# Kernel optimization log

Measured on AMD Instinct MI355X. Metric: run time of the kernel, lower is better.

Reference implementation:

```python
import jax, jax.numpy as jnp
import numpy as np

B, D, R, E, L = 8192, 2048, 64, 4, 3


def setup_inputs() -> dict:
    key = jax.random.key(0)
    ks = jax.random.split(key, 6)
    inputs = jax.random.normal(ks[0], (B, D), dtype=jnp.float32)
    # xavier-normal-ish init for low-rank factors
    U = jax.random.normal(ks[1], (L, E, D, R), dtype=jnp.float32) * (2.0 / (D + R)) ** 0.5
    V = jax.random.normal(ks[2], (L, E, D, R), dtype=jnp.float32) * (2.0 / (D + R)) ** 0.5
    C = jax.random.normal(ks[3], (L, E, R, R), dtype=jnp.float32) * (1.0 / R) ** 0.5
    gate_w = jax.random.normal(ks[4], (E, D), dtype=jnp.float32) * (1.0 / D) ** 0.5
    bias = jnp.zeros((L, D), dtype=jnp.float32)
    return {"inputs": inputs, "U": U, "V": V, "C": C, "gate_w": gate_w, "bias": bias}


def reference(inputs, U, V, C, gate_w, bias):
    x0 = inputs                      # (B, D)
    x_l = inputs
    for i in range(L):
        # gating scores per expert, softmax over experts
        gs = jax.nn.softmax(x_l @ gate_w.T, axis=-1)            # (B, E)
        # low-rank cross: tanh(V^T x) -> tanh(C .) -> U .
        vx = jnp.tanh(jnp.einsum('edr,bd->ber', V[i], x_l))     # (B, E, R)
        cx = jnp.tanh(jnp.einsum('esr,ber->bes', C[i], vx))     # (B, E, R)
        uv = jnp.einsum('eds,bes->bed', U[i], cx)               # (B, E, D)
        dot = (uv + bias[i][None, None, :]) * x0[:, None, :]    # (B, E, D)
        x_l = jnp.einsum('bed,be->bd', dot, gs) + x_l           # MoE combine + residual
    return x_l
```

## Files before the change

### kernel.cpp

```cpp
#include <hip/hip_runtime.h>
#include <cmath>

#define Bb 8192
#define Dd 2048
#define Rr 64
#define Ee 4
#define Ll 3

typedef __bf16 bf16x8 __attribute__((ext_vector_type(8)));
typedef float f32x4 __attribute__((ext_vector_type(4)));
typedef unsigned short u16x8 __attribute__((ext_vector_type(8)));
typedef unsigned short u16x4 __attribute__((ext_vector_type(4)));

__device__ __forceinline__ unsigned short f2bf(float f){
  unsigned u = __builtin_bit_cast(unsigned, f);
  u += 0x7fffu + ((u >> 16) & 1u);
  return (unsigned short)(u >> 16);
}
__device__ __forceinline__ float bf2f(unsigned short h){
  return __builtin_bit_cast(float, ((unsigned)h) << 16);
}

__global__ __launch_bounds__(256) void prep_w_k(const float* __restrict__ U,
                                                const float* __restrict__ V,
                                                const float* __restrict__ C,
                                                const float* __restrict__ gw,
                                                unsigned short* __restrict__ VfT,
                                                unsigned short* __restrict__ UfT,
                                                unsigned short* __restrict__ cb16,
                                                unsigned short* __restrict__ gw16){
  const int NV = Ll * 256 * Dd;
  const int NU = Ll * Dd * 256;
  const int NC = Ll * Ee * Rr * Rr;
  const int NG = Ee * Dd;
  const int total = NV + NU + NC + NG;
  for (int idx = blockIdx.x * blockDim.x + threadIdx.x; idx < total; idx += gridDim.x * blockDim.x){
    if (idx < NV){
      int l = idx / (256 * Dd); int rem = idx - l * 256 * Dd;
      int n = rem / Dd, d = rem - n * Dd;
      int e = n >> 6, r = n & 63;
      VfT[idx] = f2bf(V[(((size_t)l * Ee + e) * Dd + d) * Rr + r]);
    } else if (idx < NV + NU){
      int j = idx - NV;
      int l = j / (Dd * 256); int rem = j - l * Dd * 256;
      int d = rem / 256, k = rem - d * 256;
      int e = k >> 6, s = k & 63;
      UfT[j] = f2bf(U[(((size_t)l * Ee + e) * Dd + d) * Rr + s]);
    } else if (idx < NV + NU + NC){
      int j = idx - NV - NU;
      cb16[j] = f2bf(C[j]);
    } else {
      int j = idx - NV - NU - NC;
      gw16[j] = f2bf(gw[j]);
    }
  }
}

__global__ __launch_bounds__(256) void cast_gate_k(const float* __restrict__ x,
                                                   unsigned short* __restrict__ xb0,
                                                   const unsigned short* __restrict__ gw16,
                                                   float* __restrict__ gs){
  const int lane = threadIdx.x & 63;
  const int w = threadIdx.x >> 6;
  const int row = blockIdx.x * 4 + w;
  float s0 = 0.f, s1 = 0.f, s2 = 0.f, s3 = 0.f;
  #pragma unroll
  for (int c = 0; c < 4; c++){
    const int k = c * 512 + lane * 8;
    const float* xr = x + (size_t)row * Dd + k;
    f32x4 v0 = *(const f32x4*)xr;
    f32x4 v1 = *(const f32x4*)(xr + 4);
    float xf[8];
    u16x8 ob;
    #pragma unroll
    for (int u = 0; u < 4; u++){
      xf[u] = v0[u]; xf[4 + u] = v1[u];
      ob[u] = f2bf(v0[u]); ob[4 + u] = f2bf(v1[u]);
    }
    *(u16x8*)(xb0 + (size_t)row * Dd + k) = ob;
    u16x8 g0v = *(const u16x8*)(gw16 + 0 * Dd + k);
    u16x8 g1v = *(const u16x8*)(gw16 + 1 * Dd + k);
    u16x8 g2v = *(const u16x8*)(gw16 + 2 * Dd + k);
    u16x8 g3v = *(const u16x8*)(gw16 + 3 * Dd + k);
    #pragma unroll
    for (int u = 0; u < 8; u++){
      s0 += xf[u] * bf2f(g0v[u]);
      s1 += xf[u] * bf2f(g1v[u]);
      s2 += xf[u] * bf2f(g2v[u]);
      s3 += xf[u] * bf2f(g3v[u]);
    }
  }
  #pragma unroll
  for (int m = 1; m < 64; m <<= 1){
    s0 += __shfl_xor(s0, m, 64);
    s1 += __shfl_xor(s1, m, 64);
    s2 += __shfl_xor(s2, m, 64);
    s3 += __shfl_xor(s3, m, 64);
  }
  if (lane == 0){
    float mx = fmaxf(fmaxf(s0, s1), fmaxf(s2, s3));
    float e0 = __expf(s0 - mx), e1 = __expf(s1 - mx), e2 = __expf(s2 - mx), e3 = __expf(s3 - mx);
    float inv = 1.f / (e0 + e1 + e2 + e3);
    f32x4 g; g[0] = e0 * inv; g[1] = e1 * inv; g[2] = e2 * inv; g[3] = e3 * inv;
    *(f32x4*)(gs + (size_t)row * 4) = g;
  }
}

__global__ __launch_bounds__(256) void gate_k(const float* __restrict__ xv,
                                              const unsigned short* __restrict__ gw16,
                                              float* __restrict__ gs){
  const int lane = threadIdx.x & 63;
  const int w = threadIdx.x >> 6;
  const int row = blockIdx.x * 4 + w;
  float s0 = 0.f, s1 = 0.f, s2 = 0.f, s3 = 0.f;
  #pragma unroll
  for (int c = 0; c < 4; c++){
    const int k = c * 512 + lane * 8;
    const float* xr = xv + (size_t)row * Dd + k;
    f32x4 v0 = *(const f32x4*)xr;
    f32x4 v1 = *(const f32x4*)(xr + 4);
    float xf[8];
    #pragma unroll
    for (int u = 0; u < 4; u++){ xf[u] = v0[u]; xf[4 + u] = v1[u]; }
    u16x8 g0v = *(const u16x8*)(gw16 + 0 * Dd + k);
    u16x8 g1v = *(const u16x8*)(gw16 + 1 * Dd + k);
    u16x8 g2v = *(const u16x8*)(gw16 + 2 * Dd + k);
    u16x8 g3v = *(const u16x8*)(gw16 + 3 * Dd + k);
    #pragma unroll
    for (int u = 0; u < 8; u++){
      s0 += xf[u] * bf2f(g0v[u]);
      s1 += xf[u] * bf2f(g1v[u]);
      s2 += xf[u] * bf2f(g2v[u]);
      s3 += xf[u] * bf2f(g3v[u]);
    }
  }
  #pragma unroll
  for (int m = 1; m < 64; m <<= 1){
    s0 += __shfl_xor(s0, m, 64);
    s1 += __shfl_xor(s1, m, 64);
    s2 += __shfl_xor(s2, m, 64);
    s3 += __shfl_xor(s3, m, 64);
  }
  if (lane == 0){
    float mx = fmaxf(fmaxf(s0, s1), fmaxf(s2, s3));
    float e0 = __expf(s0 - mx), e1 = __expf(s1 - mx), e2 = __expf(s2 - mx), e3 = __expf(s3 - mx);
    float inv = 1.f / (e0 + e1 + e2 + e3);
    f32x4 g; g[0] = e0 * inv; g[1] = e1 * inv; g[2] = e2 * inv; g[3] = e3 * inv;
    *(f32x4*)(gs + (size_t)row * 4) = g;
  }
}

template<bool AF32>
__global__ __launch_bounds__(256) void gemm1_k(const void* __restrict__ Av,
                                               const unsigned short* __restrict__ BT,
                                               unsigned short* __restrict__ vxp){
  const int bm0 = blockIdx.x * 128;
  const int bn0 = blockIdx.y * 128;
  const int z   = blockIdx.z;
  const int kc0 = z * 512;
  const int tid = threadIdx.x;
  const int lane = tid & 63;
  const int wv = tid >> 6;
  const int wm = wv >> 1, wn = wv & 1;

  __shared__ __align__(16) char smraw[20480];
  unsigned short (*As)[40] = (unsigned short (*)[40])smraw;
  unsigned short (*Bs)[40] = (unsigned short (*)[40])(smraw + 10240);
  float (*epi)[132] = (float (*)[132])smraw;

  f32x4 acc[4][4] = {};
  const int arow = tid >> 2;
  const int aseg = tid & 3;

  const float* Af = (const float*)Av;
  const unsigned short* Ab = (const unsigned short*)Av;

  f32x4 a4[4]; u16x8 ar0, ar1;
  u16x8 br0, br1;
  if constexpr (AF32){
    a4[0] = *(const f32x4*)(Af + (size_t)(bm0 + arow) * Dd + kc0 + aseg * 8);
    a4[1] = *(const f32x4*)(Af + (size_t)(bm0 + arow) * Dd + kc0 + aseg * 8 + 4);
    a4[2] = *(const f32x4*)(Af + (size_t)(bm0 + arow + 64) * Dd + kc0 + aseg * 8);
    a4[3] = *(const f32x4*)(Af + (size_t)(bm0 + arow + 64) * Dd + kc0 + aseg * 8 + 4);
  } else {
    ar0 = *(const u16x8*)(Ab + (size_t)(bm0 + arow) * Dd + kc0 + aseg * 8);
    ar1 = *(const u16x8*)(Ab + (size_t)(bm0 + arow + 64) * Dd + kc0 + aseg * 8);
  }
  br0 = *(const u16x8*)(BT + (size_t)(bn0 + arow) * Dd + kc0 + aseg * 8);
  br1 = *(const u16x8*)(BT + (size_t)(bn0 + arow + 64) * Dd + kc0 + aseg * 8);

  for (int k0 = kc0; k0 < kc0 + 512; k0 += 32){
    __syncthreads();
    if constexpr (AF32){
      u16x8 av0, av1;
      #pragma unroll
      for (int j = 0; j < 4; j++){
        av0[j] = f2bf(a4[0][j]); av0[4 + j] = f2bf(a4[1][j]);
        av1[j] = f2bf(a4[2][j]); av1[4 + j] = f2bf(a4[3][j]);
      }
      *(u16x8*)(&As[arow][aseg * 8])      = av0;
      *(u16x8*)(&As[arow + 64][aseg * 8]) = av1;
    } else {
      *(u16x8*)(&As[arow][aseg * 8])      = ar0;
      *(u16x8*)(&As[arow + 64][aseg * 8]) = ar1;
    }
    *(u16x8*)(&Bs[arow][aseg * 8])      = br0;
    *(u16x8*)(&Bs[arow + 64][aseg * 8]) = br1;
    __syncthreads();

    int kn = k0 + 32;
    if (kn < kc0 + 512){
      if constexpr (AF32){
        a4[0] = *(const f32x4*)(Af + (size_t)(bm0 + arow) * Dd + kn + aseg * 8);
        a4[1] = *(const f32x4*)(Af + (size_t)(bm0 + arow) * Dd + kn + aseg * 8 + 4);
        a4[2] = *(const f32x4*)(Af + (size_t)(bm0 + arow + 64) * Dd + kn + aseg * 8);
        a4[3] = *(const f32x4*)(Af + (size_t)(bm0 + arow + 64) * Dd + kn + aseg * 8 + 4);
      } else {
        ar0 = *(const u16x8*)(Ab + (size_t)(bm0 + arow) * Dd + kn + aseg * 8);
        ar1 = *(const u16x8*)(Ab + (size_t)(bm0 + arow + 64) * Dd + kn + aseg * 8);
      }
      br0 = *(const u16x8*)(BT + (size_t)(bn0 + arow) * Dd + kn + aseg * 8);
      br1 = *(const u16x8*)(BT + (size_t)(bn0 + arow + 64) * Dd + kn + aseg * 8);
    }

    bf16x8 af[4];
    #pragma unroll
    for (int mi = 0; mi < 4; mi++)
      af[mi] = *reinterpret_cast<const bf16x8*>(&As[wm * 64 + mi * 16 + (lane & 15)][(lane >> 4) * 8]);
    #pragma unroll
    for (int nj = 0; nj < 4; nj++){
      bf16x8 bfr = *reinterpret_cast<const bf16x8*>(&Bs[wn * 64 + nj * 16 + (lane & 15)][(lane >> 4) * 8]);
      #pragma unroll
      for (int mi = 0; mi < 4; mi++)
        acc[mi][nj] = __builtin_amdgcn_mfma_f32_16x16x32_bf16(af[mi], bfr, acc[mi][nj], 0, 0, 0);
    }
  }

  unsigned short* outz = vxp + (size_t)z * Bb * 256;
  #pragma unroll
  for (int h = 0; h < 4; h++){
    __syncthreads();
    if (wm == (h >> 1)){
      const int mib = (h & 1) * 2;
      #pragma unroll
      for (int m2 = 0; m2 < 2; m2++)
        #pragma unroll
        for (int nj = 0; nj < 4; nj++)
          #pragma unroll
          for (int q = 0; q < 4; q++)
            epi[m2 * 16 + (lane >> 4) * 4 + q][wn * 64 + nj * 16 + (lane & 15)] = acc[mib + m2][nj][q];
    }
    __syncthreads();
    #pragma unroll
    for (int c = 0; c < 2; c++){
      int idx = c * 256 + tid;
      int r = idx >> 4;
      int col = (idx & 15) * 8;
      f32x4 v0 = *(const f32x4*)&epi[r][col];
      f32x4 v1 = *(const f32x4*)&epi[r][col + 4];
      u16x8 ov;
      #pragma unroll
      for (int j = 0; j < 4; j++){ ov[j] = f2bf(v0[j]); ov[4 + j] = f2bf(v1[j]); }
      *(u16x8*)(outz + (size_t)(bm0 + h * 32 + r) * 256 + bn0 + col) = ov;
    }
  }
}

template<bool FROMPLOG>
__global__ __launch_bounds__(256) void gemm2_k(const unsigned short* __restrict__ vxp,
                                               const unsigned short* __restrict__ cb,
                                               const float* __restrict__ gsb,
                                               const float* __restrict__ plog,
                                               unsigned short* __restrict__ wb){
  const int bm0 = blockIdx.x * 64;
  const int e   = blockIdx.y;
  const int tid = threadIdx.x;
  const int lane = tid & 63;
  const int wv = tid >> 6;
  const int wm = wv >> 1, wn = wv & 1;

  __shared__ __align__(16) char smraw[19456];
  unsigned short (*As)[72] = (unsigned short (*)[72])smraw;
  unsigned short (*Bs)[72] = (unsigned short (*)[72])(smraw + 9216);
  float (*gs_l)[4] = (float (*)[4])(smraw + 18432);
  unsigned short (*epi)[72] = (unsigned short (*)[72])smraw;

  if constexpr (FROMPLOG){
    int r = tid >> 2, q = tid & 3;
    f32x4 s = {0.f, 0.f, 0.f, 0.f};
    #pragma unroll
    for (int ci = 0; ci < 4; ci++)
      s += *(const f32x4*)(plog + ((size_t)(q * 4 + ci) * Bb + bm0 + r) * 4);
    #pragma unroll
    for (int j = 0; j < 4; j++){
      s[j] += __shfl_xor(s[j], 1, 64);
      s[j] += __shfl_xor(s[j], 2, 64);
    }
    if (q == 0){
      float mx = fmaxf(fmaxf(s[0], s[1]), fmaxf(s[2], s[3]));
      float e0 = __expf(s[0] - mx), e1 = __expf(s[1] - mx), e2 = __expf(s[2] - mx), e3 = __expf(s[3] - mx);
      float inv = 1.f / (e0 + e1 + e2 + e3);
      f32x4 g; g[0] = e0 * inv; g[1] = e1 * inv; g[2] = e2 * inv; g[3] = e3 * inv;
      *(f32x4*)&gs_l[r][0] = g;
    }
  } else {
    if (tid < 64) *(f32x4*)&gs_l[tid][0] = *(const f32x4*)(gsb + (size_t)(bm0 + tid) * 4);
  }

  const int arow = tid >> 2;
  const int aseg = tid & 3;

  float tv[16];
  #pragma unroll
  for (int j = 0; j < 16; j++) tv[j] = 0.f;
  #pragma unroll
  for (int z = 0; z < 4; z++){
    const unsigned short* vz = vxp + ((size_t)z * Bb + bm0 + arow) * 256 + e * 64 + aseg * 16;
    u16x8 p0 = *(const u16x8*)vz;
    u16x8 p1 = *(const u16x8*)(vz + 8);
    #pragma unroll
    for (int j = 0; j < 8; j++){ tv[j] += bf2f(p0[j]); tv[8 + j] += bf2f(p1[j]); }
  }
  u16x8 av0, av1;
  #pragma unroll
  for (int j = 0; j < 4; j++){
    av0[j] = f2bf(tanhf(tv[j]));     av0[4 + j] = f2bf(tanhf(tv[4 + j]));
    av1[j] = f2bf(tanhf(tv[8 + j])); av1[4 + j] = f2bf(tanhf(tv[12 + j]));
  }
  *(u16x8*)(&As[arow][aseg * 16]) = av0;
  *(u16x8*)(&As[arow][aseg * 16 + 8]) = av1;
  *(u16x8*)(&Bs[arow][aseg * 16])     = *(const u16x8*)(cb + e * 4096 + arow * 64 + aseg * 16);
  *(u16x8*)(&Bs[arow][aseg * 16 + 8]) = *(const u16x8*)(cb + e * 4096 + arow * 64 + aseg * 16 + 8);
  __syncthreads();

  f32x4 acc[2][2] = {};
  #pragma unroll
  for (int kk = 0; kk < 2; kk++){
    bf16x8 af[2];
    #pragma unroll
    for (int mi = 0; mi < 2; mi++)
      af[mi] = *reinterpret_cast<const bf16x8*>(&As[wm * 32 + mi * 16 + (lane & 15)][kk * 32 + (lane >> 4) * 8]);
    #pragma unroll
    for (int nj = 0; nj < 2; nj++){
      bf16x8 bfr = *reinterpret_cast<const bf16x8*>(&Bs[wn * 32 + nj * 16 + (lane & 15)][kk * 32 + (lane >> 4) * 8]);
      #pragma unroll
      for (int mi = 0; mi < 2; mi++)
        acc[mi][nj] = __builtin_amdgcn_mfma_f32_16x16x32_bf16(af[mi], bfr, acc[mi][nj], 0, 0, 0);
    }
  }

  __syncthreads();
  #pragma unroll
  for (int mi = 0; mi < 2; mi++)
    #pragma unroll
    for (int nj = 0; nj < 2; nj++)
      #pragma unroll
      for (int q = 0; q < 4; q++){
        int row = wm * 32 + mi * 16 + (lane >> 4) * 4 + q;
        int col = wn * 32 + nj * 16 + (lane & 15);
        float g = gs_l[row][e];
        epi[row][col] = f2bf(g * tanhf(acc[mi][nj][q]));
      }
  __syncthreads();
  #pragma unroll
  for (int c = 0; c < 2; c++){
    int idx = c * 256 + tid;
    int row = idx >> 3;
    int col = (idx & 7) * 8;
    *(u16x8*)(wb + (size_t)(bm0 + row) * 256 + e * 64 + col) = *(const u16x8*)(&epi[row][col]);
  }
}

template<int MODE, bool X0BF>
__global__ __launch_bounds__(256, 4) void gemm3_k(const unsigned short* __restrict__ A,
                                                  const unsigned short* __restrict__ BT,
                                                  const float* __restrict__ x0f,
                                                  const unsigned short* __restrict__ x0b,
                                                  unsigned short* __restrict__ xst,
                                                  const float* __restrict__ biasrow,
                                                  float* __restrict__ out,
                                                  const unsigned short* __restrict__ gw16,
                                                  float* __restrict__ plog){
  const int bm0 = blockIdx.x * 128;
  const int bn0 = blockIdx.y * 128;
  const int tid = threadIdx.x;
  const int lane = tid & 63;
  const int wv = tid >> 6;
  const int wm = wv >> 1, wn = wv & 1;

  __shared__ __align__(16) char smraw[20480];
  unsigned short (*As)[40] = (unsigned short (*)[40])smraw;
  unsigned short (*Bs)[40] = (unsigned short (*)[40])(smraw + 10240);
  float (*epi)[132] = (float (*)[132])smraw;

  f32x4 acc[4][4] = {};
  const int arow = tid >> 2;
  const int aseg = tid & 3;

  u16x8 ar0 = *(const u16x8*)(A + (size_t)(bm0 + arow) * 256 + aseg * 8);
  u16x8 ar1 = *(const u16x8*)(A + (size_t)(bm0 + arow + 64) * 256 + aseg * 8);
  u16x8 br0 = *(const u16x8*)(BT + (size_t)(bn0 + arow) * 256 + aseg * 8);
  u16x8 br1 = *(const u16x8*)(BT + (size_t)(bn0 + arow + 64) * 256 + aseg * 8);

  for (int k0 = 0; k0 < 256; k0 += 32){
    __syncthreads();
    *(u16x8*)(&As[arow][aseg * 8])      = ar0;
    *(u16x8*)(&As[arow + 64][aseg * 8]) = ar1;
    *(u16x8*)(&Bs[arow][aseg * 8])      = br0;
    *(u16x8*)(&Bs[arow + 64][aseg * 8]) = br1;
    __syncthreads();
    if (k0 + 32 < 256){
      ar0 = *(const u16x8*)(A + (size_t)(bm0 + arow) * 256 + k0 + 32 + aseg * 8);
      ar1 = *(const u16x8*)(A + (size_t)(bm0 + arow + 64) * 256 + k0 + 32 + aseg * 8);
      br0 = *(const u16x8*)(BT + (size_t)(bn0 + arow) * 256 + k0 + 32 + aseg * 8);
      br1 = *(const u16x8*)(BT + (size_t)(bn0 + arow + 64) * 256 + k0 + 32 + aseg * 8);
    }
    bf16x8 af[4];
    #pragma unroll
    for (int mi = 0; mi < 4; mi++)
      af[mi] = *reinterpret_cast<const bf16x8*>(&As[wm * 64 + mi * 16 + (lane & 15)][(lane >> 4) * 8]);
    #pragma unroll
    for (int nj = 0; nj < 4; nj++){
      bf16x8 bfr = *reinterpret_cast<const bf16x8*>(&Bs[wn * 64 + nj * 16 + (lane & 15)][(lane >> 4) * 8]);
      #pragma unroll
      for (int mi = 0; mi < 4; mi++)
        acc[mi][nj] = __builtin_amdgcn_mfma_f32_16x16x32_bf16(af[mi], bfr, acc[mi][nj], 0, 0, 0);
    }
  }

  #pragma unroll
  for (int h = 0; h < 4; h++){
    __syncthreads();
    if (wm == (h >> 1)){
      const int mib = (h & 1) * 2;
      #pragma unroll
      for (int m2 = 0; m2 < 2; m2++)
        #pragma unroll
        for (int nj = 0; nj < 4; nj++)
          #pragma unroll
          for (int q = 0; q < 4; q++)
            epi[m2 * 16 + (lane >> 4) * 4 + q][wn * 64 + nj * 16 + (lane & 15)] = acc[mib + m2][nj][q];
    }
    __syncthreads();
    #pragma unroll
    for (int c = 0; c < 4; c++){
      int idx = c * 256 + tid;
      int r = idx >> 5;
      int col = (idx & 31) * 4;
      int row = bm0 + h * 32 + r;
      size_t o = (size_t)row * Dd + bn0 + col;
      f32x4 y = *(const f32x4*)&epi[r][col];
      f32x4 bv = *(const f32x4*)(biasrow + bn0 + col);
      f32x4 x0v;
      if constexpr (X0BF){
        u16x4 xv = *(const u16x4*)(x0b + o);
        #pragma unroll
        for (int j = 0; j < 4; j++) x0v[j] = bf2f(xv[j]);
      } else {
        x0v = *(const f32x4*)(x0f + o);
      }
      f32x4 xo;
      if constexpr (MODE == 0){
        xo = x0v;
      } else {
        u16x4 xv = *(const u16x4*)(xst + o);
        #pragma unroll
        for (int j = 0; j < 4; j++) xo[j] = bf2f(xv[j]);
      }
      f32x4 xn;
      #pragma unroll
      for (int j = 0; j < 4; j++) xn[j] = xo[j] + x0v[j] * (bv[j] + y[j]);
      if constexpr (MODE == 2){
        *(f32x4*)(out + o) = xn;
      } else {
        u16x4 xnb;
        #pragma unroll
        for (int j = 0; j < 4; j++) xnb[j] = f2bf(xn[j]);
        *(u16x4*)(xst + o) = xnb;
      }
      if constexpr (MODE != 2){
        float s[4];
        #pragma unroll
        for (int e = 0; e < 4; e++){
          u16x4 gv = *(const u16x4*)(gw16 + (size_t)e * Dd + bn0 + col);
          s[e] = xn[0] * bf2f(gv[0]) + xn[1] * bf2f(gv[1])
               + xn[2] * bf2f(gv[2]) + xn[3] * bf2f(gv[3]);
        }
        #pragma unroll
        for (int m = 1; m < 32; m <<= 1)
          #pragma unroll
          for (int e = 0; e < 4; e++) s[e] += __shfl_xor(s[e], m, 64);
        if ((tid & 31) == 0){
          f32x4 pv; pv[0] = s[0]; pv[1] = s[1]; pv[2] = s[2]; pv[3] = s[3];
          *(f32x4*)(plog + ((size_t)blockIdx.y * Bb + row) * 4) = pv;
        }
      }
    }
  }
}

extern "C" void kernel_launch(void* const* d_in, const int* in_sizes, int n_in,
                              void* d_out, int out_size, void* d_ws, size_t ws_size,
                              hipStream_t stream){
  (void)in_sizes; (void)n_in; (void)out_size;
  const float* inp  = (const float*)d_in[0];
  const float* U    = (const float*)d_in[1];
  const float* V    = (const float*)d_in[2];
  const float* C    = (const float*)d_in[3];
  const float* gw   = (const float*)d_in[4];
  const float* bias = (const float*)d_in[5];
  float* out = (float*)d_out;

  char* ws = (char*)d_ws;
  size_t o = 0;
  unsigned short* xb  = (unsigned short*)(ws + o); o += (size_t)Bb * Dd * 2;
  unsigned short* vxp = (unsigned short*)(ws + o); o += (size_t)4 * Bb * 256 * 2;
  unsigned short* wb  = (unsigned short*)(ws + o); o += (size_t)Bb * 256 * 2;
  float*          gsb = (float*)(ws + o);          o += (size_t)Bb * 4 * 4;
  float*          plog= (float*)(ws + o);          o += (size_t)16 * Bb * 4 * 4;
  unsigned short* vft = (unsigned short*)(ws + o); o += (size_t)Ll * 256 * Dd * 2;
  unsigned short* uft = (unsigned short*)(ws + o); o += (size_t)Ll * Dd * 256 * 2;
  unsigned short* cb16= (unsigned short*)(ws + o); o += (size_t)Ll * Ee * Rr * Rr * 2;
  unsigned short* g16 = (unsigned short*)(ws + o); o += (size_t)Ee * Dd * 2;
  if (ws_size < o) return;
  unsigned short* x0b = nullptr;
  if (ws_size >= o + (size_t)Bb * Dd * 2){
    x0b = (unsigned short*)(ws + o); o += (size_t)Bb * Dd * 2;
  }
  const bool hx = (x0b != nullptr);

  prep_w_k<<<1024, 256, 0, stream>>>(U, V, C, gw, vft, uft, cb16, g16);
  if (hx) cast_gate_k<<<Bb / 4, 256, 0, stream>>>(inp, x0b, g16, gsb);

  for (int l = 0; l < Ll; l++){
    const unsigned short* vftl = vft + (size_t)l * 256 * Dd;
    const unsigned short* uftl = uft + (size_t)l * Dd * 256;
    const unsigned short* cbl  = cb16 + (size_t)l * Ee * Rr * Rr;
    const float* biasl = bias + (size_t)l * Dd;

    if (l == 0){
      if (hx){
        gemm1_k<false><<<dim3(Bb / 128, 2, 4), 256, 0, stream>>>(x0b, vftl, vxp);
      } else {
        gate_k<<<Bb / 4, 256, 0, stream>>>(inp, g16, gsb);
        gemm1_k<true><<<dim3(Bb / 128, 2, 4), 256, 0, stream>>>(inp, vftl, vxp);
      }
      gemm2_k<false><<<dim3(Bb / 64, Ee), 256, 0, stream>>>(vxp, cbl, gsb, plog, wb);
    } else {
      gemm1_k<false><<<dim3(Bb / 128, 2, 4), 256, 0, stream>>>(xb, vftl, vxp);
      gemm2_k<true><<<dim3(Bb / 64, Ee), 256, 0, stream>>>(vxp, cbl, gsb, plog, wb);
    }

    dim3 g3(Bb / 128, Dd / 128);
    if (l == 0){
      if (hx) gemm3_k<0, true ><<<g3, 256, 0, stream>>>(wb, uftl, inp, x0b, xb, biasl, out, g16, plog);
      else    gemm3_k<0, false><<<g3, 256, 0, stream>>>(wb, uftl, inp, x0b, xb, biasl, out, g16, plog);
    } else if (l == 1){
      if (hx) gemm3_k<1, true ><<<g3, 256, 0, stream>>>(wb, uftl, inp, x0b, xb, biasl, out, g16, plog);
      else    gemm3_k<1, false><<<g3, 256, 0, stream>>>(wb, uftl, inp, x0b, xb, biasl, out, g16, plog);
    } else {
      if (hx) gemm3_k<2, true ><<<g3, 256, 0, stream>>>(wb, uftl, inp, x0b, xb, biasl, out, g16, plog);
      else    gemm3_k<2, false><<<g3, 256, 0, stream>>>(wb, uftl, inp, x0b, xb, biasl, out, g16, plog);
    }
  }
}
```

Measured before the change: 209.4 us.

## Fuse layer-0 input cast and gate logits into first low-rank GEMM

Drops the standalone cast_gate_k pass. The layer-0 gemm1 now reads the fp32 input directly, converts it to bf16, and writes x0b from the bn0==0 blocks. Those same blocks accumulate per-K-chunk gate logit partials into plog, and gemm2 reduces them and applies the softmax. This removes one full read of the input and one kernel launch, at the cost of extra work and register pressure in half of the gemm1 blocks.

```diff
diff --git a/kernel.cpp b/kernel.cpp
--- a/kernel.cpp
+++ b/kernel.cpp
@@ -56,56 +56,6 @@
   }
 }
 
-__global__ __launch_bounds__(256) void cast_gate_k(const float* __restrict__ x,
-                                                   unsigned short* __restrict__ xb0,
-                                                   const unsigned short* __restrict__ gw16,
-                                                   float* __restrict__ gs){
-  const int lane = threadIdx.x & 63;
-  const int w = threadIdx.x >> 6;
-  const int row = blockIdx.x * 4 + w;
-  float s0 = 0.f, s1 = 0.f, s2 = 0.f, s3 = 0.f;
-  #pragma unroll
-  for (int c = 0; c < 4; c++){
-    const int k = c * 512 + lane * 8;
-    const float* xr = x + (size_t)row * Dd + k;
-    f32x4 v0 = *(const f32x4*)xr;
-    f32x4 v1 = *(const f32x4*)(xr + 4);
-    float xf[8];
-    u16x8 ob;
-    #pragma unroll
-    for (int u = 0; u < 4; u++){
-      xf[u] = v0[u]; xf[4 + u] = v1[u];
-      ob[u] = f2bf(v0[u]); ob[4 + u] = f2bf(v1[u]);
-    }
-    *(u16x8*)(xb0 + (size_t)row * Dd + k) = ob;
-    u16x8 g0v = *(const u16x8*)(gw16 + 0 * Dd + k);
-    u16x8 g1v = *(const u16x8*)(gw16 + 1 * Dd + k);
-    u16x8 g2v = *(const u16x8*)(gw16 + 2 * Dd + k);
-    u16x8 g3v = *(const u16x8*)(gw16 + 3 * Dd + k);
-    #pragma unroll
-    for (int u = 0; u < 8; u++){
-      s0 += xf[u] * bf2f(g0v[u]);
-      s1 += xf[u] * bf2f(g1v[u]);
-      s2 += xf[u] * bf2f(g2v[u]);
-      s3 += xf[u] * bf2f(g3v[u]);
-    }
-  }
-  #pragma unroll
-  for (int m = 1; m < 64; m <<= 1){
-    s0 += __shfl_xor(s0, m, 64);
-    s1 += __shfl_xor(s1, m, 64);
-    s2 += __shfl_xor(s2, m, 64);
-    s3 += __shfl_xor(s3, m, 64);
-  }
-  if (lane == 0){
-    float mx = fmaxf(fmaxf(s0, s1), fmaxf(s2, s3));
-    float e0 = __expf(s0 - mx), e1 = __expf(s1 - mx), e2 = __expf(s2 - mx), e3 = __expf(s3 - mx);
-    float inv = 1.f / (e0 + e1 + e2 + e3);
-    f32x4 g; g[0] = e0 * inv; g[1] = e1 * inv; g[2] = e2 * inv; g[3] = e3 * inv;
-    *(f32x4*)(gs + (size_t)row * 4) = g;
-  }
-}
-
 __global__ __launch_bounds__(256) void gate_k(const float* __restrict__ xv,
                                               const unsigned short* __restrict__ gw16,
                                               float* __restrict__ gs){
@@ -150,10 +100,13 @@
   }
 }
 
-template<bool AF32>
+template<int M1>
 __global__ __launch_bounds__(256) void gemm1_k(const void* __restrict__ Av,
                                                const unsigned short* __restrict__ BT,
-                                               unsigned short* __restrict__ vxp){
+                                               unsigned short* __restrict__ vxp,
+                                               unsigned short* __restrict__ x0b,
+                                               const unsigned short* __restrict__ gw16,
+                                               float* __restrict__ plog){
   const int bm0 = blockIdx.x * 128;
   const int bn0 = blockIdx.y * 128;
   const int z   = blockIdx.z;
@@ -174,10 +127,14 @@
 
   const float* Af = (const float*)Av;
   const unsigned short* Ab = (const unsigned short*)Av;
+  const bool dog = (M1 == 1) && (bn0 == 0);
+
+  float sg0[4] = {0.f, 0.f, 0.f, 0.f};
+  float sg1[4] = {0.f, 0.f, 0.f, 0.f};
 
   f32x4 a4[4]; u16x8 ar0, ar1;
   u16x8 br0, br1;
-  if constexpr (AF32){
+  if constexpr (M1 != 0){
     a4[0] = *(const f32x4*)(Af + (size_t)(bm0 + arow) * Dd + kc0 + aseg * 8);
     a4[1] = *(const f32x4*)(Af + (size_t)(bm0 + arow) * Dd + kc0 + aseg * 8 + 4);
     a4[2] = *(const f32x4*)(Af + (size_t)(bm0 + arow + 64) * Dd + kc0 + aseg * 8);
@@ -191,7 +148,7 @@
 
   for (int k0 = kc0; k0 < kc0 + 512; k0 += 32){
     __syncthreads();
-    if constexpr (AF32){
+    if constexpr (M1 != 0){
       u16x8 av0, av1;
       #pragma unroll
       for (int j = 0; j < 4; j++){
@@ -200,6 +157,12 @@
       }
       *(u16x8*)(&As[arow][aseg * 8])      = av0;
       *(u16x8*)(&As[arow + 64][aseg * 8]) = av1;
+      if constexpr (M1 == 1){
+        if (dog){
+          *(u16x8*)(x0b + (size_t)(bm0 + arow) * Dd + k0 + aseg * 8)      = av0;
+          *(u16x8*)(x0b + (size_t)(bm0 + arow + 64) * Dd + k0 + aseg * 8) = av1;
+        }
+      }
     } else {
       *(u16x8*)(&As[arow][aseg * 8])      = ar0;
       *(u16x8*)(&As[arow + 64][aseg * 8]) = ar1;
@@ -208,9 +171,26 @@
     *(u16x8*)(&Bs[arow + 64][aseg * 8]) = br1;
     __syncthreads();
 
+    if constexpr (M1 == 1){
+      if (dog){
+        u16x8 g0v = *(const u16x8*)(gw16 + (size_t)0 * Dd + k0 + aseg * 8);
+        u16x8 g1v = *(const u16x8*)(gw16 + (size_t)1 * Dd + k0 + aseg * 8);
+        u16x8 g2v = *(const u16x8*)(gw16 + (size_t)2 * Dd + k0 + aseg * 8);
+        u16x8 g3v = *(const u16x8*)(gw16 + (size_t)3 * Dd + k0 + aseg * 8);
+        #pragma unroll
+        for (int u = 0; u < 8; u++){
+          float xa = (u < 4) ? a4[0][u] : a4[1][u - 4];
+          float xc = (u < 4) ? a4[2][u] : a4[3][u - 4];
+          float g0 = bf2f(g0v[u]), g1 = bf2f(g1v[u]), g2 = bf2f(g2v[u]), g3 = bf2f(g3v[u]);
+          sg0[0] += xa * g0; sg0[1] += xa * g1; sg0[2] += xa * g2; sg0[3] += xa * g3;
+          sg1[0] += xc * g0; sg1[1] += xc * g1; sg1[2] += xc * g2; sg1[3] += xc * g3;
+        }
+      }
+    }
+
     int kn = k0 + 32;
     if (kn < kc0 + 512){
-      if constexpr (AF32){
+      if constexpr (M1 != 0){
         a4[0] = *(const f32x4*)(Af + (size_t)(bm0 + arow) * Dd + kn + aseg * 8);
         a4[1] = *(const f32x4*)(Af + (size_t)(bm0 + arow) * Dd + kn + aseg * 8 + 4);
         a4[2] = *(const f32x4*)(Af + (size_t)(bm0 + arow + 64) * Dd + kn + aseg * 8);
@@ -236,6 +216,22 @@
     }
   }
 
+  if constexpr (M1 == 1){
+    if (dog){
+      #pragma unroll
+      for (int e = 0; e < 4; e++){
+        sg0[e] += __shfl_xor(sg0[e], 1, 64); sg0[e] += __shfl_xor(sg0[e], 2, 64);
+        sg1[e] += __shfl_xor(sg1[e], 1, 64); sg1[e] += __shfl_xor(sg1[e], 2, 64);
+      }
+      if (aseg == 0){
+        f32x4 p0; p0[0] = sg0[0]; p0[1] = sg0[1]; p0[2] = sg0[2]; p0[3] = sg0[3];
+        f32x4 p1; p1[0] = sg1[0]; p1[1] = sg1[1]; p1[2] = sg1[2]; p1[3] = sg1[3];
+        *(f32x4*)(plog + ((size_t)z * Bb + bm0 + arow) * 4) = p0;
+        *(f32x4*)(plog + ((size_t)z * Bb + bm0 + arow + 64) * 4) = p1;
+      }
+    }
+  }
+
   unsigned short* outz = vxp + (size_t)z * Bb * 256;
   #pragma unroll
   for (int h = 0; h < 4; h++){
@@ -266,7 +262,7 @@
   }
 }
 
-template<bool FROMPLOG>
+template<int NPART>
 __global__ __launch_bounds__(256) void gemm2_k(const unsigned short* __restrict__ vxp,
                                                const unsigned short* __restrict__ cb,
                                                const float* __restrict__ gsb,
@@ -285,12 +281,12 @@
   float (*gs_l)[4] = (float (*)[4])(smraw + 18432);
   unsigned short (*epi)[72] = (unsigned short (*)[72])smraw;
 
-  if constexpr (FROMPLOG){
+  if constexpr (NPART > 0){
     int r = tid >> 2, q = tid & 3;
     f32x4 s = {0.f, 0.f, 0.f, 0.f};
     #pragma unroll
-    for (int ci = 0; ci < 4; ci++)
-      s += *(const f32x4*)(plog + ((size_t)(q * 4 + ci) * Bb + bm0 + r) * 4);
+    for (int ci = 0; ci < NPART / 4; ci++)
+      s += *(const f32x4*)(plog + ((size_t)(q * (NPART / 4) + ci) * Bb + bm0 + r) * 4);
     #pragma unroll
     for (int j = 0; j < 4; j++){
       s[j] += __shfl_xor(s[j], 1, 64);
@@ -530,7 +526,6 @@
   const bool hx = (x0b != nullptr);
 
   prep_w_k<<<1024, 256, 0, stream>>>(U, V, C, gw, vft, uft, cb16, g16);
-  if (hx) cast_gate_k<<<Bb / 4, 256, 0, stream>>>(inp, x0b, g16, gsb);
 
   for (int l = 0; l < Ll; l++){
     const unsigned short* vftl = vft + (size_t)l * 256 * Dd;
@@ -540,15 +535,16 @@
 
     if (l == 0){
       if (hx){
-        gemm1_k<false><<<dim3(Bb / 128, 2, 4), 256, 0, stream>>>(x0b, vftl, vxp);
+        gemm1_k<1><<<dim3(Bb / 128, 2, 4), 256, 0, stream>>>(inp, vftl, vxp, x0b, g16, plog);
+        gemm2_k<4><<<dim3(Bb / 64, Ee), 256, 0, stream>>>(vxp, cbl, gsb, plog, wb);
       } else {
         gate_k<<<Bb / 4, 256, 0, stream>>>(inp, g16, gsb);
-        gemm1_k<true><<<dim3(Bb / 128, 2, 4), 256, 0, stream>>>(inp, vftl, vxp);
-      }
-      gemm2_k<false><<<dim3(Bb / 64, Ee), 256, 0, stream>>>(vxp, cbl, gsb, plog, wb);
+        gemm1_k<2><<<dim3(Bb / 128, 2, 4), 256, 0, stream>>>(inp, vftl, vxp, nullptr, g16, plog);
+        gemm2_k<0><<<dim3(Bb / 64, Ee), 256, 0, stream>>>(vxp, cbl, gsb, plog, wb);
+      }
     } else {
-      gemm1_k<false><<<dim3(Bb / 128, 2, 4), 256, 0, stream>>>(xb, vftl, vxp);
-      gemm2_k<true><<<dim3(Bb / 64, Ee), 256, 0, stream>>>(vxp, cbl, gsb, plog, wb);
+      gemm1_k<0><<<dim3(Bb / 128, 2, 4), 256, 0, stream>>>(xb, vftl, vxp, nullptr, g16, plog);
+      gemm2_k<16><<<dim3(Bb / 64, Ee), 256, 0, stream>>>(vxp, cbl, gsb, plog, wb);
     }
 
     dim3 g3(Bb / 128, Dd / 128);
```

New measurement: 208.6 us. No clear change (-0.4%).
